# Performance work log

Measured on AMD Instinct MI355X. Metric: run time of the kernel, lower is better.

The kernel has to match this reference:

```python
import jax, jax.numpy as jnp
import numpy as np

K = 3
GROUPS = K * K
PAD = 1


def setup_inputs() -> dict:
    key = jax.random.key(0)
    k1, k2 = jax.random.split(key)
    B, C_in, H, W = 32, 256, 64, 64
    C_out = 512  # pointwise in/out channels (out_channels incl. missing)
    x = jax.random.normal(k1, (B, C_in, H, W), dtype=jnp.float32)
    # pointwise 1x1 conv weight [out, in] (no bias), kaiming-ish scale
    w_pw = jax.random.normal(k2, (C_out, C_out), dtype=jnp.float32) / np.sqrt(C_out)
    return {"x": x, "w_pw": w_pw}


def _shift_conv(x, out_full):
    """Grouped one-hot shift conv + centre-channel padding. Returns (B, out_full, H, W)."""
    B, C, H, W = x.shape
    in_ch = C - C % GROUPS            # 252
    in_cpg = in_ch // GROUPS          # 28
    out_ch = out_full - out_full % GROUPS  # 504
    out_cpg = out_ch // GROUPS        # 56
    miss = out_full - out_ch          # 8

    # one-hot kernel broadcasts over the group's input channels -> per-group channel sum
    s = x[:, :in_ch].reshape(B, GROUPS, in_cpg, H, W).sum(axis=2)  # (B, 9, H, W)
    sp = jnp.pad(s, ((0, 0), (0, 0), (PAD, PAD), (PAD, PAD)))
    offsets = [(i, j) for i in range(K) for j in range(K)]
    # group g output = padded group-sum shifted by (i, j); stride 1 -> same HxW
    shifts = jnp.stack(
        [sp[:, g, i:i + H, j:j + W] for g, (i, j) in enumerate(offsets)], axis=1
    )  # (B, 9, H, W)
    # every channel within a group is identical
    out = jnp.repeat(shifts, out_cpg, axis=1)  # (B, 504, H, W)
    if miss > 0:
        centre = out[:, out_ch // 2:out_ch // 2 + 1]  # (B, 1, H, W)
        out = jnp.concatenate(
            [out, jnp.broadcast_to(centre, (B, miss, H, W))], axis=1
        )  # (B, 512, H, W)
    return out


def reference(x, w_pw):
    out_full = w_pw.shape[0]
    shifted = jax.lax.stop_gradient(_shift_conv(x, out_full))  # torch.no_grad()
    # 1x1 pointwise conv, no bias
    return jnp.einsum('oc,bchw->bohw', w_pw, shifted)
```

## Files before the change

kernel.cpp:

```cpp
#include <hip/hip_runtime.h>

#define B_   32
#define CIN  256
#define H_   64
#define W_   64
#define COUT 512
#define G_   9
#define CPG_IN  28
#define HW_  (H_*W_)
#define HW4_ (HW_/4)

typedef float f4 __attribute__((ext_vector_type(4)));

__global__ __launch_bounds__(64) void reduce_w_kernel(const float* __restrict__ w,
                                                      float* __restrict__ v) {
    const int o = blockIdx.x;
    const int t = threadIdx.x;
    const float* row = w + o * COUT;
#pragma unroll
    for (int g = 0; g < G_; ++g) {
        float val = (t < 56) ? row[g * 56 + t] : 0.0f;
        if (g == 4 && t >= 56) val = row[504 + (t - 56)];
#pragma unroll
        for (int off = 32; off; off >>= 1) val += __shfl_down(val, off);
        if (t == 0) v[o * G_ + g] = val;
    }
}

__global__ __launch_bounds__(256) void group_sum_kernel(const float* __restrict__ x,
                                                        float* __restrict__ s) {
    const int idx = blockIdx.x * 256 + threadIdx.x;
    const int hw = idx & (HW4_ - 1);
    const int gb = idx >> 10;
    const int g  = gb % G_;
    const int b  = gb / G_;
    const f4* xp = (const f4*)x;
    long base = ((long)(b * CIN + g * CPG_IN)) * HW4_ + hw;
    f4 acc = (f4)0.0f;
#pragma unroll
    for (int k = 0; k < CPG_IN; ++k) {
        acc += __builtin_nontemporal_load(xp + base + (long)k * HW4_);
    }
    ((f4*)s)[idx] = acc;
}

#define O_TILE 16
#define H_TILE 16
#define SROWS  (H_TILE + 2)
#define SCOLS  67
#define SUSED  66

__global__ __launch_bounds__(256) void shift_pw_kernel(const float* __restrict__ s,
                                                       const float* __restrict__ v,
                                                       float* __restrict__ out) {
    __shared__ float sl[G_][SROWS][SCOLS];

    const int bid = blockIdx.x;
    const int ot  = bid & 31;
    const int ht  = (bid >> 5) & 3;
    const int b   = bid >> 7;
    const int h0  = ht * H_TILE;
    const int tid = threadIdx.x;
    const int o0  = ot * O_TILE;

    const float* sb = s + (long)b * G_ * HW_;
#pragma unroll
    for (int g = 0; g < G_; ++g) {
        for (int i = tid; i < SROWS * SUSED; i += 256) {
            int r  = i / SUSED;
            int wc = i - r * SUSED;
            int gh = h0 - 1 + r;
            int gw = wc - 1;
            float val = 0.0f;
            if ((unsigned)gh < (unsigned)H_ && (unsigned)gw < (unsigned)W_)
                val = sb[g * HW_ + gh * W_ + gw];
            sl[g][r][wc] = val;
        }
    }
    __syncthreads();

    const int w0 = (tid & 15) * 4;
    const int hl = tid >> 4;

    f4 acc[O_TILE];
#pragma unroll
    for (int oi = 0; oi < O_TILE; ++oi) acc[oi] = (f4)0.0f;

#pragma unroll
    for (int g = 0; g < G_; ++g) {
        const int gi = g / 3, gj = g % 3;
        const float s0 = sl[g][hl + gi][w0 + gj + 0];
        const float s1 = sl[g][hl + gi][w0 + gj + 1];
        const float s2 = sl[g][hl + gi][w0 + gj + 2];
        const float s3 = sl[g][hl + gi][w0 + gj + 3];
#pragma unroll
        for (int oi = 0; oi < O_TILE; ++oi) {
            const float vv = v[(o0 + oi) * G_ + g];
            acc[oi].x += vv * s0;
            acc[oi].y += vv * s1;
            acc[oi].z += vv * s2;
            acc[oi].w += vv * s3;
        }
    }

    long obase = (((long)b * COUT + o0) * H_ + (h0 + hl)) * W_ + w0;
#pragma unroll
    for (int oi = 0; oi < O_TILE; ++oi) {
        __builtin_nontemporal_store(acc[oi], (f4*)(out + obase + (long)oi * HW_));
    }
}

extern "C" void kernel_launch(void* const* d_in, const int* in_sizes, int n_in,
                              void* d_out, int out_size, void* d_ws, size_t ws_size,
                              hipStream_t stream) {
    const float* x    = (const float*)d_in[0];
    const float* w_pw = (const float*)d_in[1];
    float* out = (float*)d_out;

    float* v = (float*)d_ws;
    float* s = (float*)((char*)d_ws + 32768);

    reduce_w_kernel<<<COUT, 64, 0, stream>>>(w_pw, v);

    group_sum_kernel<<<(B_ * G_ * HW4_) / 256, 256, 0, stream>>>(x, s);

    shift_pw_kernel<<<B_ * (H_ / H_TILE) * (COUT / O_TILE), 256, 0, stream>>>(s, v, out);
}
```

Baseline: 411.9 us.

## Pre-pad group-sum planes and read shift taps directly from global into registers

```diff
diff --git a/kernel.cpp b/kernel.cpp
--- a/kernel.cpp
+++ b/kernel.cpp
@@ -9,6 +9,11 @@
 #define CPG_IN  28
 #define HW_  (H_*W_)
 #define HW4_ (HW_/4)
+
+#define HP 66
+#define WP 68
+#define PLANE (HP*WP)
+#define VSTRIDE 16
 
 typedef float f4 __attribute__((ext_vector_type(4)));
 
@@ -23,38 +28,60 @@
         if (g == 4 && t >= 56) val = row[504 + (t - 56)];
 #pragma unroll
         for (int off = 32; off; off >>= 1) val += __shfl_down(val, off);
-        if (t == 0) v[o * G_ + g] = val;
+        if (t == 0) v[o * VSTRIDE + g] = val;
     }
 }
 
+#define NMAIN (B_*G_*HW4_/256)
 __global__ __launch_bounds__(256) void group_sum_kernel(const float* __restrict__ x,
                                                         float* __restrict__ s) {
-    const int idx = blockIdx.x * 256 + threadIdx.x;
-    const int hw = idx & (HW4_ - 1);
-    const int gb = idx >> 10;
-    const int g  = gb % G_;
-    const int b  = gb / G_;
-    const f4* xp = (const f4*)x;
-    long base = ((long)(b * CIN + g * CPG_IN)) * HW4_ + hw;
-    f4 acc = (f4)0.0f;
+    const int bid = blockIdx.x;
+    const int tid = threadIdx.x;
+    if (bid < NMAIN) {
+        const int idx = bid * 256 + tid;
+        const int m  = idx & (HW4_ - 1);
+        const int gb = idx >> 10;
+        const int g  = gb % G_;
+        const int b  = gb / G_;
+        const int hh = m >> 4;
+        const int ww = (m & 15) * 4;
+        const f4* xp = (const f4*)x;
+        long base = ((long)(b * CIN + g * CPG_IN)) * HW4_ + m;
+        f4 acc = (f4)0.0f;
 #pragma unroll
-    for (int k = 0; k < CPG_IN; ++k) {
-        acc += __builtin_nontemporal_load(xp + base + (long)k * HW4_);
+        for (int k = 0; k < CPG_IN; ++k) {
+            acc += __builtin_nontemporal_load(xp + base + (long)k * HW4_);
+        }
+        float* sp = s + (long)gb * PLANE + (hh + 1) * WP + (ww + 1);
+        sp[0] = acc.x; sp[1] = acc.y; sp[2] = acc.z; sp[3] = acc.w;
+    } else {
+        const int plane = bid - NMAIN;
+        float* sp = s + (long)plane * PLANE;
+#pragma unroll
+        for (int pass = 0; pass < 2; ++pass) {
+            int i = tid + pass * 256;
+            if (i < 392) {
+                int p;
+                if (i < 68)       p = i;
+                else if (i < 136) p = 65 * WP + (i - 68);
+                else {
+                    int k = i - 136;
+                    int r = 1 + (k >> 2);
+                    int c = k & 3;
+                    p = r * WP + (c == 0 ? 0 : 64 + c);
+                }
+                sp[p] = 0.0f;
+            }
+        }
     }
-    ((f4*)s)[idx] = acc;
 }
 
 #define O_TILE 16
 #define H_TILE 16
-#define SROWS  (H_TILE + 2)
-#define SCOLS  67
-#define SUSED  66
 
-__global__ __launch_bounds__(256) void shift_pw_kernel(const float* __restrict__ s,
-                                                       const float* __restrict__ v,
-                                                       float* __restrict__ out) {
-    __shared__ float sl[G_][SROWS][SCOLS];
-
+__global__ __launch_bounds__(256, 4) void shift_pw_kernel(const float* __restrict__ s,
+                                                          const float* __restrict__ v,
+                                                          float* __restrict__ out) {
     const int bid = blockIdx.x;
     const int ot  = bid & 31;
     const int ht  = (bid >> 5) & 3;
@@ -62,51 +89,38 @@
     const int h0  = ht * H_TILE;
     const int tid = threadIdx.x;
     const int o0  = ot * O_TILE;
+    const int w0  = (tid & 15) * 4;
+    const int hl  = tid >> 4;
 
-    const float* sb = s + (long)b * G_ * HW_;
+    const float* sb = s + (long)b * G_ * PLANE;
+    f4 sa[G_], sbv[G_];
 #pragma unroll
     for (int g = 0; g < G_; ++g) {
-        for (int i = tid; i < SROWS * SUSED; i += 256) {
-            int r  = i / SUSED;
-            int wc = i - r * SUSED;
-            int gh = h0 - 1 + r;
-            int gw = wc - 1;
-            float val = 0.0f;
-            if ((unsigned)gh < (unsigned)H_ && (unsigned)gw < (unsigned)W_)
-                val = sb[g * HW_ + gh * W_ + gw];
-            sl[g][r][wc] = val;
-        }
-    }
-    __syncthreads();
-
-    const int w0 = (tid & 15) * 4;
-    const int hl = tid >> 4;
-
-    f4 acc[O_TILE];
-#pragma unroll
-    for (int oi = 0; oi < O_TILE; ++oi) acc[oi] = (f4)0.0f;
-
-#pragma unroll
-    for (int g = 0; g < G_; ++g) {
-        const int gi = g / 3, gj = g % 3;
-        const float s0 = sl[g][hl + gi][w0 + gj + 0];
-        const float s1 = sl[g][hl + gi][w0 + gj + 1];
-        const float s2 = sl[g][hl + gi][w0 + gj + 2];
-        const float s3 = sl[g][hl + gi][w0 + gj + 3];
-#pragma unroll
-        for (int oi = 0; oi < O_TILE; ++oi) {
-            const float vv = v[(o0 + oi) * G_ + g];
-            acc[oi].x += vv * s0;
-            acc[oi].y += vv * s1;
-            acc[oi].z += vv * s2;
-            acc[oi].w += vv * s3;
-        }
+        const int gi = g / 3;
+        const float* rp = sb + g * PLANE + (h0 + hl + gi) * WP + w0;
+        sa[g]  = *(const f4*)rp;
+        sbv[g] = *(const f4*)(rp + 4);
     }
 
     long obase = (((long)b * COUT + o0) * H_ + (h0 + hl)) * W_ + w0;
+    const float* vp = v + o0 * VSTRIDE;
 #pragma unroll
     for (int oi = 0; oi < O_TILE; ++oi) {
-        __builtin_nontemporal_store(acc[oi], (f4*)(out + obase + (long)oi * HW_));
+        f4 acc = (f4)0.0f;
+#pragma unroll
+        for (int g = 0; g < G_; ++g) {
+            const int gj = g - (g / 3) * 3;
+            const float vv = vp[oi * VSTRIDE + g];
+            float s0, s1, s2, s3;
+            if (gj == 0)      { s0 = sa[g].x; s1 = sa[g].y; s2 = sa[g].z; s3 = sa[g].w; }
+            else if (gj == 1) { s0 = sa[g].y; s1 = sa[g].z; s2 = sa[g].w; s3 = sbv[g].x; }
+            else              { s0 = sa[g].z; s1 = sa[g].w; s2 = sbv[g].x; s3 = sbv[g].y; }
+            acc.x += vv * s0;
+            acc.y += vv * s1;
+            acc.z += vv * s2;
+            acc.w += vv * s3;
+        }
+        __builtin_nontemporal_store(acc, (f4*)(out + obase + (long)oi * HW_));
     }
 }
 
@@ -122,7 +136,7 @@
 
     reduce_w_kernel<<<COUT, 64, 0, stream>>>(w_pw, v);
 
-    group_sum_kernel<<<(B_ * G_ * HW4_) / 256, 256, 0, stream>>>(x, s);
+    group_sum_kernel<<<NMAIN + B_ * G_, 256, 0, stream>>>(x, s);
 
     shift_pw_kernel<<<B_ * (H_ / H_TILE) * (COUT / O_TILE), 256, 0, stream>>>(s, v, out);
 }
```

Result: faster. 360.0 us (-12.6%).

## Fuse group-sum into shift-pointwise kernel with halo recompute per tile

Applied to the files above, without the earlier changes.

```diff
diff --git a/kernel.cpp b/kernel.cpp
--- a/kernel.cpp
+++ b/kernel.cpp
@@ -9,6 +9,7 @@
 #define CPG_IN  28
 #define HW_  (H_*W_)
 #define HW4_ (HW_/4)
+#define VSTRIDE 16
 
 typedef float f4 __attribute__((ext_vector_type(4)));
 
@@ -23,90 +24,75 @@
         if (g == 4 && t >= 56) val = row[504 + (t - 56)];
 #pragma unroll
         for (int off = 32; off; off >>= 1) val += __shfl_down(val, off);
-        if (t == 0) v[o * G_ + g] = val;
+        if (t == 0) v[o * VSTRIDE + g] = val;
     }
 }
 
-__global__ __launch_bounds__(256) void group_sum_kernel(const float* __restrict__ x,
-                                                        float* __restrict__ s) {
-    const int idx = blockIdx.x * 256 + threadIdx.x;
-    const int hw = idx & (HW4_ - 1);
-    const int gb = idx >> 10;
-    const int g  = gb % G_;
-    const int b  = gb / G_;
-    const f4* xp = (const f4*)x;
-    long base = ((long)(b * CIN + g * CPG_IN)) * HW4_ + hw;
-    f4 acc = (f4)0.0f;
-#pragma unroll
-    for (int k = 0; k < CPG_IN; ++k) {
-        acc += __builtin_nontemporal_load(xp + base + (long)k * HW4_);
-    }
-    ((f4*)s)[idx] = acc;
-}
+#define NBC (B_ * 8 * 2)
 
-#define O_TILE 16
-#define H_TILE 16
-#define SROWS  (H_TILE + 2)
-#define SCOLS  67
-#define SUSED  66
-
-__global__ __launch_bounds__(256) void shift_pw_kernel(const float* __restrict__ s,
-                                                       const float* __restrict__ v,
-                                                       float* __restrict__ out) {
-    __shared__ float sl[G_][SROWS][SCOLS];
+__global__ __launch_bounds__(256, 2) void fused_bc_kernel(const float* __restrict__ x,
+                                                          const float* __restrict__ v,
+                                                          float* __restrict__ out) {
+    __shared__ float sl[G_][10][44];
 
     const int bid = blockIdx.x;
-    const int ot  = bid & 31;
-    const int ht  = (bid >> 5) & 3;
-    const int b   = bid >> 7;
-    const int h0  = ht * H_TILE;
+    const int wh = bid & 1;
+    const int ht = (bid >> 1) & 7;
+    const int b  = bid >> 4;
+    const int h0 = ht * 8;
+    const int w0 = wh * 32;
     const int tid = threadIdx.x;
-    const int o0  = ot * O_TILE;
 
-    const float* sb = s + (long)b * G_ * HW_;
+#pragma unroll 1
+    for (int i = 0; i < 4; ++i) {
+        const int idx = tid + i * 256;
+        if (idx >= 900) break;
+        const int g   = idx / 100;
+        const int rem = idx - g * 100;
+        const int r   = rem / 10;
+        const int c4  = rem - r * 10;
+        const int gh  = h0 - 1 + r;
+        const int gc  = w0 - 4 + c4 * 4;
+        f4 acc = (f4)0.0f;
+        if ((unsigned)gh < (unsigned)H_ && (unsigned)gc < (unsigned)W_) {
+            const f4* xp = (const f4*)x + (long)(b * CIN + g * CPG_IN) * HW4_
+                         + gh * (W_ / 4) + (gc >> 2);
 #pragma unroll
-    for (int g = 0; g < G_; ++g) {
-        for (int i = tid; i < SROWS * SUSED; i += 256) {
-            int r  = i / SUSED;
-            int wc = i - r * SUSED;
-            int gh = h0 - 1 + r;
-            int gw = wc - 1;
-            float val = 0.0f;
-            if ((unsigned)gh < (unsigned)H_ && (unsigned)gw < (unsigned)W_)
-                val = sb[g * HW_ + gh * W_ + gw];
-            sl[g][r][wc] = val;
+            for (int k = 0; k < CPG_IN; ++k)
+                acc += __builtin_nontemporal_load(xp + (long)k * HW4_);
         }
+        *(f4*)&sl[g][r][c4 * 4] = acc;
     }
     __syncthreads();
 
-    const int w0 = (tid & 15) * 4;
-    const int hl = tid >> 4;
+    const int wc    = tid & 7;
+    const int hl    = (tid >> 3) & 7;
+    const int o_sub = tid >> 6;
+    const int wl    = wc * 4;
 
-    f4 acc[O_TILE];
-#pragma unroll
-    for (int oi = 0; oi < O_TILE; ++oi) acc[oi] = (f4)0.0f;
-
+    float sv[G_][4];
 #pragma unroll
     for (int g = 0; g < G_; ++g) {
-        const int gi = g / 3, gj = g % 3;
-        const float s0 = sl[g][hl + gi][w0 + gj + 0];
-        const float s1 = sl[g][hl + gi][w0 + gj + 1];
-        const float s2 = sl[g][hl + gi][w0 + gj + 2];
-        const float s3 = sl[g][hl + gi][w0 + gj + 3];
+        const int gi = g / 3, gj = g - (g / 3) * 3;
 #pragma unroll
-        for (int oi = 0; oi < O_TILE; ++oi) {
-            const float vv = v[(o0 + oi) * G_ + g];
-            acc[oi].x += vv * s0;
-            acc[oi].y += vv * s1;
-            acc[oi].z += vv * s2;
-            acc[oi].w += vv * s3;
-        }
+        for (int j = 0; j < 4; ++j)
+            sv[g][j] = sl[g][hl + gi][wl + gj + 3 + j];
     }
 
-    long obase = (((long)b * COUT + o0) * H_ + (h0 + hl)) * W_ + w0;
+    long obase = (((long)b * COUT + o_sub * 128) * H_ + (h0 + hl)) * W_ + w0 + wl;
+    const float* vp = v + (o_sub * 128) * VSTRIDE;
+#pragma unroll 4
+    for (int oi = 0; oi < 128; ++oi) {
+        f4 acc = (f4)0.0f;
 #pragma unroll
-    for (int oi = 0; oi < O_TILE; ++oi) {
-        __builtin_nontemporal_store(acc[oi], (f4*)(out + obase + (long)oi * HW_));
+        for (int g = 0; g < G_; ++g) {
+            const float vv = vp[oi * VSTRIDE + g];
+            acc.x += vv * sv[g][0];
+            acc.y += vv * sv[g][1];
+            acc.z += vv * sv[g][2];
+            acc.w += vv * sv[g][3];
+        }
+        __builtin_nontemporal_store(acc, (f4*)(out + obase + (long)oi * HW_));
     }
 }
 
@@ -118,11 +104,8 @@
     float* out = (float*)d_out;
 
     float* v = (float*)d_ws;
-    float* s = (float*)((char*)d_ws + 32768);
 
     reduce_w_kernel<<<COUT, 64, 0, stream>>>(w_pw, v);
 
-    group_sum_kernel<<<(B_ * G_ * HW4_) / 256, 256, 0, stream>>>(x, s);
-
-    shift_pw_kernel<<<B_ * (H_ / H_TILE) * (COUT / O_TILE), 256, 0, stream>>>(s, v, out);
+    fused_bc_kernel<<<NBC, 256, 0, stream>>>(x, v, out);
 }
```

After: 418.2 us. Within noise of the previous version (+1.5%).
